# Performance work log

Measured on AMD Instinct MI355X. Metric: run time of the kernel, lower is better.

## Reference

```python
import jax, jax.numpy as jnp
import numpy as np
from jax import lax

B, C, W, H, K = 4, 32, 256, 256, 9
CENTER = K // 2
EXTEND = 1.0
EPS = 1e-5


def conv2d(x, w, b, stride=(1, 1), padding='SAME'):
    y = lax.conv_general_dilated(x, w, stride, padding,
                                 dimension_numbers=('NCHW', 'OIHW', 'NCHW'))
    return y + b[None, :, None, None]


def group_norm(x, scale, bias, groups):
    b, c, h, w = x.shape
    xg = x.reshape(b, groups, c // groups, h, w)
    mu = xg.mean(axis=(2, 3, 4), keepdims=True)
    var = xg.var(axis=(2, 3, 4), keepdims=True)
    xn = ((xg - mu) * lax.rsqrt(var + EPS)).reshape(b, c, h, w)
    return xn * scale[None, :, None, None] + bias[None, :, None, None]


def bilinear_sample(feat, py, px):
    # feat: (C, W, H); py, px: (W*K, H) pixel coords, already clamped in-range
    y0 = jnp.floor(py)
    x0 = jnp.floor(px)
    wy = py - y0
    wx = px - x0
    y0i = jnp.clip(y0, 0, W - 1).astype(jnp.int32)
    y1i = jnp.clip(y0 + 1, 0, W - 1).astype(jnp.int32)
    x0i = jnp.clip(x0, 0, H - 1).astype(jnp.int32)
    x1i = jnp.clip(x0 + 1, 0, H - 1).astype(jnp.int32)
    v00 = feat[:, y0i, x0i]
    v01 = feat[:, y0i, x1i]
    v10 = feat[:, y1i, x0i]
    v11 = feat[:, y1i, x1i]
    return (v00 * (1 - wy) * (1 - wx) + v01 * (1 - wy) * wx
            + v10 * wy * (1 - wx) + v11 * wy * wx)


def ds_conv(x, w_off, b_off, gn_off_scale, gn_off_bias, w_dsc, b_dsc, gn_scale, gn_bias):
    # offset branch: conv3x3 -> GroupNorm(K groups, 2K ch) -> tanh
    off = jnp.tanh(group_norm(conv2d(x, w_off, b_off), gn_off_scale, gn_off_bias, K))
    y_off = off[:, :K]  # (B, K, W, H); x-half of offsets unused when morph == 0
    # cumulative offset scan outward from center tap (center tap offset is 0)
    low = jnp.flip(jnp.cumsum(jnp.flip(y_off[:, :CENTER], 1), 1), 1)
    up = jnp.cumsum(y_off[:, CENTER + 1:], 1)
    y_cum = jnp.concatenate([low, jnp.zeros_like(y_off[:, :1]), up], axis=1)
    # coordinate maps (morph == 0: kernel spreads along x, offsets bend y)
    y_new = jnp.arange(W, dtype=x.dtype)[None, None, :, None] + y_cum * EXTEND
    x_new = (jnp.arange(H, dtype=x.dtype)[None, None, None, :]
             + jnp.linspace(-CENTER, CENTER, K, dtype=x.dtype)[None, :, None, None])
    x_new = jnp.broadcast_to(x_new, y_new.shape)
    gy = y_new.transpose(0, 2, 1, 3).reshape(-1, W * K, H)  # 'b k w h -> b (w k) h'
    gx = x_new.transpose(0, 2, 1, 3).reshape(-1, W * K, H)
    # normalize as torch grid_sample (align_corners=True) with clamp to [-1, 1]
    gy = jnp.clip(gy / W * 2 - 1, -1.0, 1.0)
    gx = jnp.clip(gx / H * 2 - 1, -1.0, 1.0)
    py = (gy + 1) * 0.5 * (W - 1)
    px = (gx + 1) * 0.5 * (H - 1)
    deformed = jax.vmap(bilinear_sample)(x, py, px)  # (B, C, W*K, H)
    out = conv2d(deformed, w_dsc, b_dsc, stride=(K, 1), padding='VALID')  # (B, C, W, H)
    out = group_norm(out, gn_scale, gn_bias, C // 4)
    return jax.nn.relu(out)


def setup_inputs() -> dict:
    key = jax.random.key(0)
    ks = jax.random.split(key, 3)
    return {
        'input': jax.random.normal(ks[0], (B, C, W, H), jnp.float32),
        'w_off': jax.random.normal(ks[1], (2 * K, C, 3, 3), jnp.float32) * 0.05,
        'b_off': jnp.zeros((2 * K,), jnp.float32),
        'gn_off_scale': jnp.ones((2 * K,), jnp.float32),
        'gn_off_bias': jnp.zeros((2 * K,), jnp.float32),
        'w_dsc': jax.random.normal(ks[2], (C, C, K, 1), jnp.float32) * 0.05,
        'b_dsc': jnp.zeros((C,), jnp.float32),
        'gn_scale': jnp.ones((C,), jnp.float32),
        'gn_bias': jnp.zeros((C,), jnp.float32),
    }


def reference(input, w_off, b_off, gn_off_scale, gn_off_bias, w_dsc, b_dsc, gn_scale, gn_bias):
    # in_channels == out_channels so input_adjust is Identity
    return ds_conv(input, w_off, b_off, gn_off_scale, gn_off_bias, w_dsc, b_dsc, gn_scale, gn_bias)
```

## Files before the change

kernel.cpp:

```cpp
#include <hip/hip_runtime.h>
#include <hip/hip_bf16.h>

#define BB 4
#define CC 32
#define WW 256
#define HH 256
#define WH (WW*HH)

typedef __attribute__((ext_vector_type(8))) short bf16x8;
typedef __attribute__((ext_vector_type(4))) short bf16x4;
typedef __attribute__((ext_vector_type(4))) float f32x4;

typedef __attribute__((address_space(1))) const void gvoid;
typedef __attribute__((address_space(3))) void lvoid;

__device__ __forceinline__ short f2bf(float x) {
    union { float f; unsigned u; } a; a.f = x;
    unsigned r = (a.u + 0x7FFF + ((a.u >> 16) & 1)) >> 16;
    return (short)r;
}

__global__ void k0_init(const float* __restrict__ w_dsc, const float* __restrict__ w_off,
                        unsigned short* __restrict__ B3f, unsigned short* __restrict__ B8f,
                        unsigned short* __restrict__ B1f, unsigned short* __restrict__ B18f,
                        float* __restrict__ stats1, float* __restrict__ stats2) {
    int i = blockIdx.x * 256 + threadIdx.x;
    if (i < 8192) {
        int j = i & 7, l = (i >> 3) & 63, nt = (i >> 9) & 1, ch = i >> 10;
        int o = nt * 16 + (l & 15);
        int kl = ((l >> 4) << 3) | j;
        int tap = kl >> 2, cl = kl & 3;
        B3f[i] = (unsigned short)f2bf(w_dsc[(o * 32 + ch * 4 + cl) * 9 + tap]);
    } else if (i < 9216) {
        int e = i - 8192;
        int j = e & 7, l = (e >> 3) & 63, nt = e >> 9;
        int o = nt * 16 + (l & 15);
        int k8 = ((l >> 4) << 3) | j;
        B8f[e] = (unsigned short)f2bf(w_dsc[(o * 32 + k8) * 9 + 8]);
    } else if (i < 13312) {
        int e = i - 9216;
        int j = e & 7, l = (e >> 3) & 63, ch = e >> 9;
        int o = l & 15;
        int kl = ((l >> 4) << 3) | j;
        int tap = kl >> 2, cl = kl & 3;
        B1f[e] = (o < 10) ? (unsigned short)f2bf(w_off[(o * 32 + ch * 4 + cl) * 9 + tap]) : 0;
    } else if (i < 13824) {
        int e = i - 13312;
        int j = e & 7, l = (e >> 3) & 63;
        int o = l & 15;
        int k8 = ((l >> 4) << 3) | j;
        B18f[e] = (o < 10) ? (unsigned short)f2bf(w_off[(o * 32 + k8) * 9 + 8]) : 0;
    }
    if (i < 40) stats1[i] = 0.f;
    if (i < 64) stats2[i] = 0.f;
}

__global__ __launch_bounds__(256, 2) void k1_conv(
    const float* __restrict__ x, const unsigned short* __restrict__ B1f,
    const unsigned short* __restrict__ B18f, const float* __restrict__ b_off,
    float* __restrict__ off_buf, float* __restrict__ stats1) {
    __shared__ __align__(16) unsigned short tbf[8 * 4 * 136 * 4];
    __shared__ float scr[40];
    __shared__ __align__(16) short Apan[16 * 64 * 8];
    __shared__ __align__(16) short A8pan[16 * 64 * 8];

    const int b = blockIdx.z;
    const int w0 = blockIdx.y * 2;
    const int h0 = blockIdx.x * 128;
    const int p = threadIdx.x;
    const int lane = p & 63;
    const int wv = p >> 6;
    const int hl = p & 127;
    const int wi = p >> 7;
    const int mt = p >> 4;
    const int mrow = p & 15;

    const float* xb = x + (size_t)b * CC * WH;

#pragma unroll
    for (int u = 0; u < 5; ++u) {
        if (u < 4 || p < 64) {
            int s = p + u * 256;
            int g = s / 136;
            int rem = s - g * 136;
            int r = rem / 34;
            int k = rem - r * 34;
            int y = w0 - 1 + r;
            int g0 = h0 - 4 + (k << 2);
            f32x4 v0 = {0.f,0.f,0.f,0.f}, v1 = v0, v2 = v0, v3 = v0;
            if (y >= 0 && y < 256 && g0 >= 0 && g0 <= 252) {
                const float* bp2 = xb + y * 256 + g0;
                v0 = *(const f32x4*)(bp2 + (size_t)(g * 4 + 0) * WH);
                v1 = *(const f32x4*)(bp2 + (size_t)(g * 4 + 1) * WH);
                v2 = *(const f32x4*)(bp2 + (size_t)(g * 4 + 2) * WH);
                v3 = *(const f32x4*)(bp2 + (size_t)(g * 4 + 3) * WH);
            }
            int base = ((g * 4 + r) * 136 + (k << 2)) * 4;
#pragma unroll
            for (int i = 0; i < 4; ++i) {
                bf16x4 pv;
                pv[0] = f2bf(v0[i]); pv[1] = f2bf(v1[i]);
                pv[2] = f2bf(v2[i]); pv[3] = f2bf(v3[i]);
                *(bf16x4*)&tbf[base + i * 4] = pv;
            }
        }
    }

    bf16x8 Bf[8], B8g;
    {
        const bf16x8* bp = (const bf16x8*)B1f;
#pragma unroll
        for (int ch = 0; ch < 8; ++ch) Bf[ch] = bp[ch * 64 + lane];
        B8g = ((const bf16x8*)B18f)[lane];
    }

    f32x4 acc[4];
#pragma unroll
    for (int i = 0; i < 4; ++i) acc[i] = (f32x4){0.f, 0.f, 0.f, 0.f};

    __syncthreads();

#pragma unroll
    for (int ch = 0; ch < 8; ++ch) {
#pragma unroll
        for (int kg = 0; kg < 4; ++kg) {
            bf16x4 lo, hi;
            {
                int tap = kg * 2, dy = tap / 3, dx = tap - dy * 3;
                lo = *(const bf16x4*)&tbf[((ch * 4 + wi + dy) * 136 + hl + dx + 3) * 4];
            }
            {
                int tap = kg * 2 + 1, dy = tap / 3, dx = tap - dy * 3;
                hi = *(const bf16x4*)&tbf[((ch * 4 + wi + dy) * 136 + hl + dx + 3) * 4];
            }
            bf16x8 pv;
#pragma unroll
            for (int e = 0; e < 4; ++e) { pv[e] = lo[e]; pv[4 + e] = hi[e]; }
            *(bf16x8*)&Apan[mt * 512 + (kg * 16 + mrow) * 8] = pv;
        }
        {
            bf16x4 pv8 = *(const bf16x4*)&tbf[((ch * 4 + wi + 2) * 136 + hl + 5) * 4];
            *(bf16x4*)&A8pan[mt * 512 + ((ch >> 1) * 16 + mrow) * 8 + (ch & 1) * 4] = pv8;
        }
        __syncthreads();

#pragma unroll
        for (int i = 0; i < 4; ++i) {
            bf16x8 a = *(const bf16x8*)&Apan[((wv * 4 + i) * 64 + lane) * 8];
            acc[i] = __builtin_amdgcn_mfma_f32_16x16x32_bf16(a, Bf[ch], acc[i], 0, 0, 0);
        }
        __syncthreads();
    }
#pragma unroll
    for (int i = 0; i < 4; ++i) {
        bf16x8 a = *(const bf16x8*)&A8pan[((wv * 4 + i) * 64 + lane) * 8];
        acc[i] = __builtin_amdgcn_mfma_f32_16x16x32_bf16(a, B8g, acc[i], 0, 0, 0);
    }

    const int oc = lane & 15;
    float bias = (oc < 10) ? b_off[oc] : 0.f;
#pragma unroll
    for (int i = 0; i < 4; ++i)
#pragma unroll
        for (int r = 0; r < 4; ++r) acc[i][r] += bias;

    if (oc < 10) {
#pragma unroll
        for (int i = 0; i < 4; ++i) {
            int px = (wv * 4 + i) * 16 + (lane >> 4) * 4;
            size_t addr = (size_t)(b * 10 + oc) * WH +
                          (size_t)(w0 + (px >> 7)) * 256 + h0 + (px & 127);
            *(f32x4*)&off_buf[addr] = acc[i];
        }
    }

    float s = 0.f, q = 0.f;
#pragma unroll
    for (int i = 0; i < 4; ++i)
#pragma unroll
        for (int r = 0; r < 4; ++r) { float v = acc[i][r]; s += v; q += v * v; }
    s += __shfl_xor(s, 1, 64);  q += __shfl_xor(q, 1, 64);
    s += __shfl_xor(s, 16, 64); q += __shfl_xor(q, 16, 64);
    s += __shfl_xor(s, 32, 64); q += __shfl_xor(q, 32, 64);
    __syncthreads();
    if (lane < 10 && !(lane & 1)) {
        int g = lane >> 1;
        scr[(g * 2 + 0) * 4 + wv] = s;
        scr[(g * 2 + 1) * 4 + wv] = q;
    }
    __syncthreads();
    if (threadIdx.x < 10) {
        int g = threadIdx.x >> 1, which = threadIdx.x & 1;
        float sum = scr[(g * 2 + which) * 4 + 0] + scr[(g * 2 + which) * 4 + 1] +
                    scr[(g * 2 + which) * 4 + 2] + scr[(g * 2 + which) * 4 + 3];
        atomicAdd(&stats1[(b * 5 + g) * 2 + which], sum);
    }
}

__global__ __launch_bounds__(256, 2) void k3_sample(
    const float* __restrict__ xin, const float* __restrict__ off_buf,
    const float* __restrict__ stats1, const float* __restrict__ go_scale,
    const float* __restrict__ go_bias, const unsigned short* __restrict__ B3f,
    const unsigned short* __restrict__ B8f, const float* __restrict__ b_dsc,
    float* __restrict__ pre_out, float* __restrict__ stats2) {
    __shared__ __align__(16) float tile[2][4 * 14 * 96];
    __shared__ __align__(16) short Apan[16 * 64 * 8];
    __shared__ __align__(16) short A8pan[16 * 64 * 8];

    const int b = blockIdx.z;
    const int w0 = blockIdx.y * 4;
    const int h0 = blockIdx.x * 64;
    const int p = threadIdx.x;
    const int lane = p & 63;
    const int wv = p >> 6;
    const int h = h0 + (p & 63);
    const int w = w0 + (p >> 6);
    const int mt = p >> 4;
    const int mrow = p & 15;
    const int row0 = w0 - 5;
    const int col0 = h0 - 8;

    const float* xb = xin + (size_t)b * CC * WH;

    auto dma = [&](int buf, int chn) {
#pragma unroll
        for (int u = 0; u < 6; ++u) {
            if (u < 5 || p < 64) {
                int t = p + u * 256;
                int c = t / 336;
                int rem = t - c * 336;
                int r = rem / 24;
                int cf4 = rem - r * 24;
                int y = min(max(row0 + r, 0), 255);
                int g0 = min(max(col0 + (cf4 << 2), 0), 252);
                const float* gp = xb + (size_t)(chn * 4 + c) * WH + y * 256 + g0;
                __builtin_amdgcn_global_load_lds((gvoid*)gp,
                                                 (lvoid*)&tile[buf][t * 4], 16, 0, 0);
            }
        }
    };

    dma(0, 0);

    bf16x8 Bf[8][2], B8g[2];
    {
        const bf16x8* bp = (const bf16x8*)B3f;
#pragma unroll
        for (int ch = 0; ch < 8; ++ch) {
            Bf[ch][0] = bp[(ch * 2 + 0) * 64 + lane];
            Bf[ch][1] = bp[(ch * 2 + 1) * 64 + lane];
        }
        B8g[0] = ((const bf16x8*)B8f)[lane];
        B8g[1] = ((const bf16x8*)B8f)[64 + lane];
    }

    const float INV1 = 1.f / (2.f * WH);
    float t9[9];
    size_t obase = (size_t)b * 10 * WH + (size_t)w * 256 + h;
#pragma unroll
    for (int c = 0; c < 9; ++c) {
        float v = off_buf[obase + (size_t)c * WH];
        int g = c >> 1;
        float s1 = stats1[(b * 5 + g) * 2 + 0];
        float q1 = stats1[(b * 5 + g) * 2 + 1];
        float mean = s1 * INV1;
        float istd = rsqrtf(fmaf(q1, INV1, -(mean * mean)) + 1e-5f);
        v = (v - mean) * istd * go_scale[c] + go_bias[c];
        t9[c] = tanhf(v);
    }
    float ycum[9];
    ycum[3] = t9[3];
    ycum[2] = ycum[3] + t9[2];
    ycum[1] = ycum[2] + t9[1];
    ycum[0] = ycum[1] + t9[0];
    ycum[4] = 0.f;
    ycum[5] = t9[5];
    ycum[6] = ycum[5] + t9[6];
    ycum[7] = ycum[6] + t9[7];
    ycum[8] = ycum[7] + t9[8];

    f32x4 acc[4][2];
#pragma unroll
    for (int i = 0; i < 4; ++i) {
        acc[i][0] = (f32x4){0.f, 0.f, 0.f, 0.f};
        acc[i][1] = (f32x4){0.f, 0.f, 0.f, 0.f};
    }

    const float SC = 255.f / 256.f;

#pragma unroll
    for (int ch = 0; ch < 8; ++ch) {
        asm volatile("s_waitcnt vmcnt(0)" ::: "memory");
        __builtin_amdgcn_sched_barrier(0);
        __syncthreads();
        __builtin_amdgcn_sched_barrier(0);
        if (ch < 7) dma((ch + 1) & 1, ch + 1);
        const float* tb = tile[ch & 1];

#pragma unroll
        for (int kg = 0; kg < 4; ++kg) {
            bf16x8 pv;
#pragma unroll
            for (int t = 0; t < 2; ++t) {
                int k = kg * 2 + t;
                float py = fminf(fmaxf(((float)w + ycum[k]) * SC, 0.f), 255.f);
                float pxc = fminf(fmaxf((float)(h + k - 4) * SC, 0.f), 255.f);
                float y0f = floorf(py), x0f = floorf(pxc);
                float wy = py - y0f, wx = pxc - x0f;
                int r0 = (int)y0f - row0;
                int r1 = min((int)y0f + 1, 255) - row0;
                int tc = (int)x0f - col0;
                float w00 = (1.f - wy) * (1.f - wx);
                float w01 = (1.f - wy) * wx;
                float w10 = wy * (1.f - wx);
                float w11 = wy * wx;
#pragma unroll
                for (int cl = 0; cl < 4; ++cl) {
                    const float* p0 = tb + (cl * 14 + r0) * 96 + tc;
                    const float* p1 = tb + (cl * 14 + r1) * 96 + tc;
                    float v = fmaf(w00, p0[0],
                              fmaf(w01, p0[1], fmaf(w10, p1[0], w11 * p1[1])));
                    pv[t * 4 + cl] = f2bf(v);
                }
            }
            *(bf16x8*)&Apan[mt * 512 + (kg * 16 + mrow) * 8] = pv;
        }
        {
            float py = fminf(fmaxf(((float)w + ycum[8]) * SC, 0.f), 255.f);
            float pxc = fminf(fmaxf((float)(h + 4) * SC, 0.f), 255.f);
            float y0f = floorf(py), x0f = floorf(pxc);
            float wy = py - y0f, wx = pxc - x0f;
            int r0 = (int)y0f - row0;
            int r1 = min((int)y0f + 1, 255) - row0;
            int tc = (int)x0f - col0;
            float w00 = (1.f - wy) * (1.f - wx);
            float w01 = (1.f - wy) * wx;
            float w10 = wy * (1.f - wx);
            float w11 = wy * wx;
            bf16x4 pv8;
#pragma unroll
            for (int cl = 0; cl < 4; ++cl) {
                const float* p0 = tb + (cl * 14 + r0) * 96 + tc;
                const float* p1 = tb + (cl * 14 + r1) * 96 + tc;
                float v = fmaf(w00, p0[0],
                          fmaf(w01, p0[1], fmaf(w10, p1[0], w11 * p1[1])));
                pv8[cl] = f2bf(v);
            }
            *(bf16x4*)&A8pan[mt * 512 + ((ch >> 1) * 16 + mrow) * 8 + (ch & 1) * 4] = pv8;
        }
        __syncthreads();

#pragma unroll
        for (int i = 0; i < 4; ++i) {
            bf16x8 a = *(const bf16x8*)&Apan[((wv * 4 + i) * 64 + lane) * 8];
            acc[i][0] = __builtin_amdgcn_mfma_f32_16x16x32_bf16(a, Bf[ch][0], acc[i][0], 0, 0, 0);
            acc[i][1] = __builtin_amdgcn_mfma_f32_16x16x32_bf16(a, Bf[ch][1], acc[i][1], 0, 0, 0);
        }
    }
#pragma unroll
    for (int i = 0; i < 4; ++i) {
        bf16x8 a = *(const bf16x8*)&A8pan[((wv * 4 + i) * 64 + lane) * 8];
        acc[i][0] = __builtin_amdgcn_mfma_f32_16x16x32_bf16(a, B8g[0], acc[i][0], 0, 0, 0);
        acc[i][1] = __builtin_amdgcn_mfma_f32_16x16x32_bf16(a, B8g[1], acc[i][1], 0, 0, 0);
    }

    const int oc0 = lane & 15;
    float bias0 = b_dsc[oc0];
    float bias1 = b_dsc[16 + oc0];
#pragma unroll
    for (int i = 0; i < 4; ++i)
#pragma unroll
        for (int r = 0; r < 4; ++r) { acc[i][0][r] += bias0; acc[i][1][r] += bias1; }

#pragma unroll
    for (int i = 0; i < 4; ++i) {
        int px = (wv * 4 + i) * 16 + (lane >> 4) * 4;
        size_t rowoff = (size_t)(w0 + (px >> 6)) * 256 + h0 + (px & 63);
        *(f32x4*)&pre_out[(size_t)(b * 32 + oc0) * WH + rowoff] = acc[i][0];
        *(f32x4*)&pre_out[(size_t)(b * 32 + 16 + oc0) * WH + rowoff] = acc[i][1];
    }

    float s0 = 0.f, q0 = 0.f, s1 = 0.f, q1 = 0.f;
#pragma unroll
    for (int i = 0; i < 4; ++i)
#pragma unroll
        for (int r = 0; r < 4; ++r) {
            float v0 = acc[i][0][r], v1 = acc[i][1][r];
            s0 += v0; q0 += v0 * v0; s1 += v1; q1 += v1 * v1;
        }
#pragma unroll
    for (int m = 0; m < 4; ++m) {
        int d = (m == 0) ? 1 : (m == 1) ? 2 : (m == 2) ? 16 : 32;
        s0 += __shfl_xor(s0, d, 64); q0 += __shfl_xor(q0, d, 64);
        s1 += __shfl_xor(s1, d, 64); q1 += __shfl_xor(q1, d, 64);
    }
    __syncthreads();
    float* scratch = tile[0];
    if (lane < 16 && !(lane & 3)) {
        int g = lane >> 2;
        scratch[((0 * 4 + g) * 2 + 0) * 4 + wv] = s0;
        scratch[((0 * 4 + g) * 2 + 1) * 4 + wv] = q0;
        scratch[((1 * 4 + g) * 2 + 0) * 4 + wv] = s1;
        scratch[((1 * 4 + g) * 2 + 1) * 4 + wv] = q1;
    }
    __syncthreads();
    if (threadIdx.x < 16) {
        int gg = threadIdx.x >> 1, which = threadIdx.x & 1;
        float sum = scratch[(gg * 2 + which) * 4 + 0] + scratch[(gg * 2 + which) * 4 + 1] +
                    scratch[(gg * 2 + which) * 4 + 2] + scratch[(gg * 2 + which) * 4 + 3];
        atomicAdd(&stats2[(b * 8 + gg) * 2 + which], sum);
    }
}

__global__ __launch_bounds__(256) void k5_gn(float4* __restrict__ out,
                                             const float* __restrict__ stats2,
                                             const float* __restrict__ gs,
                                             const float* __restrict__ gb) {
    int idx = blockIdx.x * 256 + threadIdx.x;
    int bo = idx >> 14;
    int b = bo >> 5;
    int o = bo & 31;
    int g = o >> 2;
    const float INV2 = 1.f / (4.f * WH);
    float s = stats2[(b * 8 + g) * 2 + 0];
    float q = stats2[(b * 8 + g) * 2 + 1];
    float mean = s * INV2;
    float istd = rsqrtf(fmaf(q, INV2, -(mean * mean)) + 1e-5f);
    float sc = gs[o] * istd;
    float bi = gb[o] - mean * sc;
    float4 v = out[idx];
    v.x = fmaxf(fmaf(v.x, sc, bi), 0.f);
    v.y = fmaxf(fmaf(v.y, sc, bi), 0.f);
    v.z = fmaxf(fmaf(v.z, sc, bi), 0.f);
    v.w = fmaxf(fmaf(v.w, sc, bi), 0.f);
    out[idx] = v;
}

extern "C" void kernel_launch(void* const* d_in, const int* in_sizes, int n_in,
                              void* d_out, int out_size, void* d_ws, size_t ws_size,
                              hipStream_t stream) {
    const float* x        = (const float*)d_in[0];
    const float* w_off    = (const float*)d_in[1];
    const float* b_off    = (const float*)d_in[2];
    const float* go_scale = (const float*)d_in[3];
    const float* go_bias  = (const float*)d_in[4];
    const float* w_dsc    = (const float*)d_in[5];
    const float* b_dsc    = (const float*)d_in[6];
    const float* gn_scale = (const float*)d_in[7];
    const float* gn_bias  = (const float*)d_in[8];
    float* out = (float*)d_out;

    float* ws = (float*)d_ws;
    float* off_buf = ws;
    unsigned short* B3f  = (unsigned short*)(ws + 2621440);
    unsigned short* B8f  = (unsigned short*)(ws + 2625536);
    unsigned short* B1f  = (unsigned short*)(ws + 2626048);
    unsigned short* B18f = (unsigned short*)(ws + 2628096);
    float* stats1 = ws + 2628352;
    float* stats2 = stats1 + 80;

    k0_init<<<54, 256, 0, stream>>>(w_dsc, w_off, B3f, B8f, B1f, B18f, stats1, stats2);
    k1_conv<<<dim3(2, 128, BB), 256, 0, stream>>>(x, B1f, B18f, b_off, off_buf, stats1);
    k3_sample<<<dim3(4, 64, BB), 256, 0, stream>>>(x, off_buf, stats1, go_scale, go_bias,
                                                   B3f, B8f, b_dsc, out, stats2);
    k5_gn<<<8192, 256, 0, stream>>>((float4*)out, stats2, gn_scale, gn_bias);
}
```

Measured before the change: 183.2 us.

## Gather MFMA A-fragments directly from LDS tile, drop staging panels and barriers

The offset-branch conv no longer stages im2col A-panels in shared memory. Each lane now computes its own tile addresses once and loads its bf16x4 halves straight from the bf16 input tile before each MFMA. This removes two shared arrays, a round of LDS writes, and two __syncthreads per channel iteration. The smaller LDS footprint allows launch bounds to rise to 4 blocks per SM, which adds register pressure and may cause more LDS bank conflicts on the direct gathers.

```diff
diff --git a/kernel.cpp b/kernel.cpp
--- a/kernel.cpp
+++ b/kernel.cpp
@@ -55,14 +55,12 @@
     if (i < 64) stats2[i] = 0.f;
 }
 
-__global__ __launch_bounds__(256, 2) void k1_conv(
+__global__ __launch_bounds__(256, 4) void k1_conv(
     const float* __restrict__ x, const unsigned short* __restrict__ B1f,
     const unsigned short* __restrict__ B18f, const float* __restrict__ b_off,
     float* __restrict__ off_buf, float* __restrict__ stats1) {
     __shared__ __align__(16) unsigned short tbf[8 * 4 * 136 * 4];
     __shared__ float scr[40];
-    __shared__ __align__(16) short Apan[16 * 64 * 8];
-    __shared__ __align__(16) short A8pan[16 * 64 * 8];
 
     const int b = blockIdx.z;
     const int w0 = blockIdx.y * 2;
@@ -70,10 +68,6 @@
     const int p = threadIdx.x;
     const int lane = p & 63;
     const int wv = p >> 6;
-    const int hl = p & 127;
-    const int wi = p >> 7;
-    const int mt = p >> 4;
-    const int mrow = p & 15;
 
     const float* xb = x + (size_t)b * CC * WH;
 
@@ -118,42 +112,42 @@
 #pragma unroll
     for (int i = 0; i < 4; ++i) acc[i] = (f32x4){0.f, 0.f, 0.f, 0.f};
 
+    const int kg = lane >> 4;
+    const int tapL = kg * 2, tapH = tapL + 1;
+    const int dyL = tapL / 3, dxL = tapL - dyL * 3;
+    const int dyH = tapH / 3, dxH = tapH - dyH * 3;
+    int loA[4], hiA[4], t8A[4];
+#pragma unroll
+    for (int i = 0; i < 4; ++i) {
+        int pp = (wv * 4 + i) * 16 + (lane & 15);
+        int hlp = pp & 127, wip = pp >> 7;
+        loA[i] = ((wip + dyL) * 136 + hlp + dxL + 3) * 4;
+        hiA[i] = ((wip + dyH) * 136 + hlp + dxH + 3) * 4;
+        t8A[i] = (((kg * 2) * 4 + wip + 2) * 136 + hlp + 5) * 4;
+    }
+
     __syncthreads();
 
 #pragma unroll
     for (int ch = 0; ch < 8; ++ch) {
-#pragma unroll
-        for (int kg = 0; kg < 4; ++kg) {
-            bf16x4 lo, hi;
-            {
-                int tap = kg * 2, dy = tap / 3, dx = tap - dy * 3;
-                lo = *(const bf16x4*)&tbf[((ch * 4 + wi + dy) * 136 + hl + dx + 3) * 4];
-            }
-            {
-                int tap = kg * 2 + 1, dy = tap / 3, dx = tap - dy * 3;
-                hi = *(const bf16x4*)&tbf[((ch * 4 + wi + dy) * 136 + hl + dx + 3) * 4];
-            }
-            bf16x8 pv;
-#pragma unroll
-            for (int e = 0; e < 4; ++e) { pv[e] = lo[e]; pv[4 + e] = hi[e]; }
-            *(bf16x8*)&Apan[mt * 512 + (kg * 16 + mrow) * 8] = pv;
-        }
-        {
-            bf16x4 pv8 = *(const bf16x4*)&tbf[((ch * 4 + wi + 2) * 136 + hl + 5) * 4];
-            *(bf16x4*)&A8pan[mt * 512 + ((ch >> 1) * 16 + mrow) * 8 + (ch & 1) * 4] = pv8;
-        }
-        __syncthreads();
-
+        const int cb = ch * 2176;
 #pragma unroll
         for (int i = 0; i < 4; ++i) {
-            bf16x8 a = *(const bf16x8*)&Apan[((wv * 4 + i) * 64 + lane) * 8];
+            bf16x4 lo = *(const bf16x4*)&tbf[cb + loA[i]];
+            bf16x4 hi = *(const bf16x4*)&tbf[cb + hiA[i]];
+            bf16x8 a;
+#pragma unroll
+            for (int e = 0; e < 4; ++e) { a[e] = lo[e]; a[4 + e] = hi[e]; }
             acc[i] = __builtin_amdgcn_mfma_f32_16x16x32_bf16(a, Bf[ch], acc[i], 0, 0, 0);
         }
-        __syncthreads();
     }
 #pragma unroll
     for (int i = 0; i < 4; ++i) {
-        bf16x8 a = *(const bf16x8*)&A8pan[((wv * 4 + i) * 64 + lane) * 8];
+        bf16x4 lo = *(const bf16x4*)&tbf[t8A[i]];
+        bf16x4 hi = *(const bf16x4*)&tbf[t8A[i] + 2176];
+        bf16x8 a;
+#pragma unroll
+        for (int e = 0; e < 4; ++e) { a[e] = lo[e]; a[4 + e] = hi[e]; }
         acc[i] = __builtin_amdgcn_mfma_f32_16x16x32_bf16(a, B8g, acc[i], 0, 0, 0);
     }
 
```

Result: no change. 181.2 us (median of 2 runs) (-1.1%).
